# Kernel optimization log

Hardware: AMD Instinct MI355X
Metric: run time of the kernel (lower is better)

Reference implementation:

```python
import jax, jax.numpy as jnp
import numpy as np

EMBED_DIM = 1024
NUM_HEADS = 16
HEAD_DIM = EMBED_DIM // NUM_HEADS
WINDOW = 128  # window_size: attend to [i-W, i+W]


def setup_inputs() -> dict:
    key = jax.random.key(0)
    ks = jax.random.split(key, 9)
    B, S, E = 4, 4096, EMBED_DIM
    s = 1.0 / np.sqrt(E)
    return {
        "x": jax.random.normal(ks[0], (B, S, E), jnp.float32),
        "Wq": jax.random.normal(ks[1], (E, E), jnp.float32) * s,
        "bq": jnp.zeros((E,), jnp.float32),
        "Wk": jax.random.normal(ks[2], (E, E), jnp.float32) * s,
        "bk": jnp.zeros((E,), jnp.float32),
        "Wv": jax.random.normal(ks[3], (E, E), jnp.float32) * s,
        "bv": jnp.zeros((E,), jnp.float32),
        "Wo": jax.random.normal(ks[4], (E, E), jnp.float32) * s,
        "bo": jnp.zeros((E,), jnp.float32),
    }


def reference(x, Wq, bq, Wk, bk, Wv, bv, Wo, bo):
    B, S, E = x.shape
    H, D, W = NUM_HEADS, HEAD_DIM, WINDOW
    scale = jnp.sqrt(jnp.asarray(D, x.dtype))

    def heads(t):  # [B,S,E] -> [B,H,S,D]
        return t.reshape(B, S, H, D).transpose(0, 2, 1, 3)

    q = heads(x @ Wq + bq)
    k = heads(x @ Wk + bk)
    v = heads(x @ Wv + bv)

    # window indices per query position: j = i + [-W..W], masked to [0, S)
    offs = jnp.arange(-W, W + 1)                 # [2W+1]
    idx = jnp.arange(S)[:, None] + offs[None, :]  # [S, 2W+1]
    valid = (idx >= 0) & (idx < S)
    idxc = jnp.clip(idx, 0, S - 1)

    k_win = k[:, :, idxc, :]  # [B,H,S,2W+1,D]
    v_win = v[:, :, idxc, :]

    scores = jnp.einsum('bhsd,bhswd->bhsw', q, k_win) / scale
    scores = jnp.where(valid[None, None], scores, jnp.asarray(-jnp.inf, scores.dtype))
    attn = jax.nn.softmax(scores, axis=-1)
    out = jnp.einsum('bhsw,bhswd->bhsd', attn, v_win)  # [B,H,S,D]

    out = out.transpose(0, 2, 1, 3).reshape(B, S, E)
    return out @ Wo + bo
```

## Files before the change

kernel.cpp:

```cpp
#include <hip/hip_runtime.h>
#include <hip/hip_bf16.h>
#include <type_traits>

typedef unsigned short u16;
typedef __attribute__((ext_vector_type(8))) short  s16x8;
typedef __attribute__((ext_vector_type(4))) short  s16x4;
typedef __attribute__((ext_vector_type(8))) __bf16 b16x8;
typedef __attribute__((ext_vector_type(4))) float  f32x4;

#define S_LEN 4096
#define NB    4
#define EMB   1024
#define NH    16
#define HD    64
#define NROWS (NB * S_LEN)
#define KDIM  1024
#define BHSTRIDE (S_LEN * HD)

static __device__ __forceinline__ u16 f2b(float f) {
  __hip_bfloat16 h = __float2bfloat16(f);
  return __builtin_bit_cast(u16, h);
}

template <typename T, typename = void>
struct mfma_takes : std::false_type {};
template <typename T>
struct mfma_takes<T, std::void_t<decltype(__builtin_amdgcn_mfma_f32_16x16x32_bf16(
    std::declval<T>(), std::declval<T>(), std::declval<f32x4>(), 0, 0, 0))>> : std::true_type {};

template <typename AB>
static __device__ __forceinline__ f32x4 mfma_any(AB a, AB b, f32x4 c) {
  return __builtin_amdgcn_mfma_f32_16x16x32_bf16(a, b, c, 0, 0, 0);
}

template <typename S8 = s16x8, typename B8 = b16x8>
static __device__ __forceinline__ f32x4 MFMA_BF16(s16x8 a, s16x8 b, f32x4 c) {
  if constexpr (mfma_takes<S8>::value)
    return mfma_any<S8>(__builtin_bit_cast(S8, a), __builtin_bit_cast(S8, b), c);
  else
    return mfma_any<B8>(__builtin_bit_cast(B8, a), __builtin_bit_cast(B8, b), c);
}

static __device__ __forceinline__ void gld_lds16(const void* g, void* l) {
  __builtin_amdgcn_global_load_lds((const __attribute__((address_space(1))) void*)g,
                                   (__attribute__((address_space(3))) void*)l, 16, 0, 0);
}

__global__ __launch_bounds__(256) void cvt_x_kernel(const float* __restrict__ in,
                                                    u16* __restrict__ out) {
  long i = ((long)blockIdx.x * 256 + threadIdx.x) * 8;
  float4 a = *(const float4*)(in + i);
  float4 b = *(const float4*)(in + i + 4);
  s16x8 o;
  o[0] = (short)f2b(a.x); o[1] = (short)f2b(a.y); o[2] = (short)f2b(a.z); o[3] = (short)f2b(a.w);
  o[4] = (short)f2b(b.x); o[5] = (short)f2b(b.y); o[6] = (short)f2b(b.z); o[7] = (short)f2b(b.w);
  *(s16x8*)(out + i) = o;
}

__global__ __launch_bounds__(256) void transpose_cvt4_kernel(
    const float* __restrict__ W0, const float* __restrict__ W1,
    const float* __restrict__ W2, const float* __restrict__ W3,
    u16* __restrict__ D0, u16* __restrict__ D1, u16* __restrict__ D2, u16* __restrict__ D3) {
  __shared__ float tile[32][33];
  const float* W; u16* D;
  switch (blockIdx.z) {
    case 0:  W = W0; D = D0; break;
    case 1:  W = W1; D = D1; break;
    case 2:  W = W2; D = D2; break;
    default: W = W3; D = D3; break;
  }
  int n0 = blockIdx.x * 32, k0 = blockIdx.y * 32;
  int tx = threadIdx.x & 31, ty = threadIdx.x >> 5;
#pragma unroll
  for (int i = ty; i < 32; i += 8)
    tile[i][tx] = W[(long)(k0 + i) * EMB + n0 + tx];
  __syncthreads();
#pragma unroll
  for (int i = ty; i < 32; i += 8)
    D[(long)(n0 + i) * EMB + k0 + tx] = f2b(tile[tx][i]);
}

#define SA_(p,k) (((p)*2+(k))*8192)
#define SB_(p,k) (32768 + ((p)*2+(k))*8192)

__global__ __launch_bounds__(512, 2) void gemm8p_kernel(
    const u16* __restrict__ A, const u16* __restrict__ Bt,
    const float* __restrict__ b0, const float* __restrict__ b1, const float* __restrict__ b2,
    void* __restrict__ Cp, u16* __restrict__ Qb, u16* __restrict__ Kp, u16* __restrict__ Vt,
    int N, int out_f32) {
  __shared__ __align__(16) u16 smem[65536];
  const int tid = threadIdx.x;
  const int w = tid >> 6, lane = tid & 63;
  const int wm = w >> 2, wn = w & 3;
  const int frow = lane & 15, fg = lane >> 4;

  const int nwg = gridDim.x;
  const int bid = ((int)blockIdx.x & 7) * (nwg >> 3) + ((int)blockIdx.x >> 3);
  const int nbn = N >> 8;
  const int bm = bid / nbn, bn = bid % nbn;

  int offA[8];
#pragma unroll
  for (int j = 0; j < 8; j++) {
    int row = wm * 128 + j * 16 + frow;
    offA[j] = row * 32 + ((fg ^ ((row ^ (row >> 2)) & 3)) << 3);
  }
  int offB[4];
#pragma unroll
  for (int j = 0; j < 4; j++) {
    int row = wn * 64 + j * 16 + frow;
    offB[j] = row * 32 + ((fg ^ ((row ^ (row >> 2)) & 3)) << 3);
  }
  int srow[2], soff[2];
#pragma unroll
  for (int L = 0; L < 2; L++) {
    int lin = L * 512 + tid;
    int r = lin >> 2;
    srow[L] = r;
    soff[L] = (((lin & 3) ^ ((r ^ (r >> 2)) & 3)) << 3);
  }
  const u16* Abase = A + (long)bm * 256 * KDIM;
  const u16* Bbase = Bt + (long)bn * 256 * KDIM;

  f32x4 acc[8][4];
#pragma unroll
  for (int m = 0; m < 8; m++)
#pragma unroll
    for (int n = 0; n < 4; n++) acc[m][n] = (f32x4)0.0f;

  auto STAGE = [&](const u16* gb, int kcol, int slot) {
#pragma unroll
    for (int L = 0; L < 2; L++)
      gld_lds16(gb + (long)srow[L] * KDIM + kcol + soff[L],
                &smem[slot + (L * 512 + w * 64) * 8]);
  };

  s16x8 af[4], bf[4];

  STAGE(Abase, 0,  SA_(0,0)); STAGE(Bbase, 0,  SB_(0,0));
  STAGE(Abase, 32, SA_(0,1)); STAGE(Bbase, 32, SB_(0,1));
  STAGE(Abase, 64, SA_(1,0)); STAGE(Bbase, 64, SB_(1,0));
  asm volatile("s_waitcnt vmcnt(4)" ::: "memory");
  asm volatile("s_barrier" ::: "memory");

#define PHASE(p, k, mh, RDB, GB, KCOL, SLOT, DOVM)                            \
  {                                                                           \
    if (RDB) {                                                                \
      _Pragma("unroll") for (int n = 0; n < 4; n++)                           \
        bf[n] = *(const s16x8*)&smem[SB_(p, k) + offB[n]];                    \
    }                                                                         \
    _Pragma("unroll") for (int m = 0; m < 4; m++)                             \
      af[m] = *(const s16x8*)&smem[SA_(p, k) + offA[(mh) * 4 + m]];           \
    STAGE(GB, KCOL, SLOT);                                                    \
    asm volatile("s_barrier" ::: "memory");                                   \
    asm volatile("s_waitcnt lgkmcnt(0)" ::: "memory");                        \
    __builtin_amdgcn_sched_barrier(0);                                        \
    __builtin_amdgcn_s_setprio(1);                                            \
    _Pragma("unroll") for (int m = 0; m < 4; m++)                             \
      _Pragma("unroll") for (int n = 0; n < 4; n++)                           \
        acc[(mh) * 4 + m][n] = MFMA_BF16(af[m], bf[n], acc[(mh) * 4 + m][n]); \
    __builtin_amdgcn_s_setprio(0);                                            \
    if (DOVM) asm volatile("s_waitcnt vmcnt(4)" ::: "memory");                \
    asm volatile("s_barrier" ::: "memory");                                   \
  }

#pragma unroll 1
  for (int i = 0; i < 8; i++) {
    const int t = 2 * i;
    const int k1 = ((t + 1) & 15) * 64;
    const int k2 = ((t + 2) & 15) * 64;
    const int k3 = ((t + 3) & 15) * 64;
    PHASE(0, 0, 0, 1, Abase, k1 + 32, SA_(1, 1), 0)
    PHASE(0, 0, 1, 0, Bbase, k1 + 32, SB_(1, 1), 0)
    PHASE(0, 1, 0, 1, Abase, k2,      SA_(0, 0), 0)
    PHASE(0, 1, 1, 0, Bbase, k2,      SB_(0, 0), 1)
    PHASE(1, 0, 0, 1, Abase, k2 + 32, SA_(0, 1), 0)
    PHASE(1, 0, 1, 0, Bbase, k2 + 32, SB_(0, 1), 0)
    PHASE(1, 1, 0, 1, Abase, k3,      SA_(1, 0), 0)
    PHASE(1, 1, 1, 0, Bbase, k3,      SB_(1, 0), 1)
  }
#undef PHASE

  asm volatile("s_waitcnt vmcnt(0)" ::: "memory");
  asm volatile("s_barrier" ::: "memory");

  const int Mbase = bm * 256 + wm * 128;

  if (!out_f32) {
    const int g = bn * 256 + wn * 64;
    const int part = g >> 10;
    const int head = (g & 1023) >> 6;
    const float* bias = (part == 0) ? b0 : ((part == 1) ? b1 : b2);
    float bv[4];
#pragma unroll
    for (int n = 0; n < 4; n++) bv[n] = bias[(g & 1023) + n * 16 + frow];
    u16* buf = &smem[w * 2048];
#pragma unroll
    for (int mf2 = 0; mf2 < 4; mf2++) {
#pragma unroll
      for (int half = 0; half < 2; half++) {
        const int mf = mf2 * 2 + half;
#pragma unroll
        for (int n = 0; n < 4; n++)
#pragma unroll
          for (int r = 0; r < 4; r++) {
            int row32 = half * 16 + 4 * fg + r;
            int col = n * 16 + frow;
            buf[row32 * 64 + (((col >> 3) ^ (row32 & 7)) << 3) + (col & 7)] =
                f2b(acc[mf][n][r] + bv[n]);
          }
      }
      asm volatile("s_waitcnt lgkmcnt(0)" ::: "memory");
      __builtin_amdgcn_sched_barrier(0);
      const int s0 = Mbase + mf2 * 32;
      if (part == 2) {
        const int d = lane;
        u16 tmp[32];
#pragma unroll
        for (int r32 = 0; r32 < 32; r32++)
          tmp[r32] = buf[r32 * 64 + (((d >> 3) ^ (r32 & 7)) << 3) + (d & 7)];
        u16* dst = Vt + ((long)((s0 >> 12) * 16 + head)) * BHSTRIDE + (long)d * S_LEN + (s0 & 4095);
#pragma unroll
        for (int q = 0; q < 4; q++) {
          s16x8 pk;
#pragma unroll
          for (int j = 0; j < 8; j++) pk[j] = (short)tmp[q * 8 + j];
          *(s16x8*)(dst + q * 8) = pk;
        }
      } else {
#pragma unroll
        for (int i = 0; i < 4; i++) {
          int flat = lane + 64 * i;
          int row32 = flat >> 3, ch = flat & 7;
          s16x8 v = *(const s16x8*)&buf[row32 * 64 + ((ch ^ (row32 & 7)) << 3)];
          int s = s0 + row32;
          u16* dst = (part == 0)
              ? (Qb + (long)s * 1024 + head * 64 + ch * 8)
              : (Kp + ((long)(s >> 12) * 16 + head) * BHSTRIDE + (long)(s & 4095) * 64 + ch * 8);
          *(s16x8*)dst = v;
        }
      }
      asm volatile("s_waitcnt lgkmcnt(0)" ::: "memory");
      __builtin_amdgcn_sched_barrier(0);
    }
  } else {
    float* fbuf = (float*)&smem[w * 2048];
    const long crow0 = (long)Mbase * N + bn * 256 + wn * 64;
#pragma unroll
    for (int mf = 0; mf < 8; mf++) {
#pragma unroll
      for (int n = 0; n < 4; n++) {
        float bvv = b0[(bn * 256 + wn * 64 + n * 16 + frow) & 1023];
#pragma unroll
        for (int r = 0; r < 4; r++) {
          int row = 4 * fg + r;
          int o = 4 * n + (frow >> 2);
          fbuf[row * 64 + ((o ^ (row & 7)) << 2) + (frow & 3)] = acc[mf][n][r] + bvv;
        }
      }
      asm volatile("s_waitcnt lgkmcnt(0)" ::: "memory");
      __builtin_amdgcn_sched_barrier(0);
#pragma unroll
      for (int i = 0; i < 4; i++) {
        int flat = lane + 64 * i;
        int row = flat >> 4, oct = lane & 15;
        float4 v = *(const float4*)&fbuf[row * 64 + ((oct ^ (row & 7)) << 2)];
        *(float4*)((float*)Cp + crow0 + (long)(mf * 16 + row) * N + oct * 4) = v;
      }
      asm volatile("s_waitcnt lgkmcnt(0)" ::: "memory");
      __builtin_amdgcn_sched_barrier(0);
    }
  }
}

#define QBLK 128

__global__ __launch_bounds__(256) void attn_kernel(const u16* __restrict__ Qb,
                                                   const u16* __restrict__ Kp,
                                                   const u16* __restrict__ Vt,
                                                   u16* __restrict__ Oa) {
  __shared__ __align__(16) u16 smem[16384];

  const int tid = threadIdx.x;
  const int w = tid >> 6, lane = tid & 63;
  const int frow = lane & 15, fg = lane >> 4;

  const int nq = S_LEN / QBLK;
  int bid = (int)blockIdx.x;
  bid = (bid & 7) * ((NB * NH * nq) >> 3) + (bid >> 3);
  const int b = bid / (NH * nq);
  const int rem = bid % (NH * nq);
  const int h = rem / nq;
  const int qt = rem % nq;
  const int q0 = qt * QBLK;
  const int qw0 = q0 + 32 * w;

  const u16* Kpb = Kp + (long)(b * NH + h) * BHSTRIDE;
  const u16* Vtb = Vt + (long)(b * NH + h) * BHSTRIDE;

  s16x8 qf[2][2];
#pragma unroll
  for (int m = 0; m < 2; m++)
#pragma unroll
    for (int kk = 0; kk < 2; kk++)
      qf[m][kk] = *(const s16x8*)(Qb + (long)(b * S_LEN + qw0 + 16 * m + frow) * 1024 +
                                  h * 64 + kk * 32 + 8 * fg);

  f32x4 acc[2][4];
#pragma unroll
  for (int m = 0; m < 2; m++)
#pragma unroll
    for (int n = 0; n < 4; n++) acc[m][n] = (f32x4)0.0f;
  float mrow[2] = {-1e30f, -1e30f};
  float lrow[2] = {0.f, 0.f};

  const int r8 = lane >> 3;
  const int cs = ((lane & 7) ^ r8) << 3;

  auto STAGE = [&](int kvb, int bufi) {
#pragma unroll
    for (int pass = 0; pass < 2; pass++) {
      int rbase = pass * 32 + w * 8;
      gld_lds16(Kpb + (long)(kvb + rbase + r8) * 64 + cs, &smem[bufi * 4096 + rbase * 64]);
      gld_lds16(Vtb + (long)(rbase + r8) * S_LEN + kvb + cs, &smem[8192 + bufi * 4096 + rbase * 64]);
    }
  };

  const int tlo = (q0 == 0) ? 2 : 0;
  const int thi = (q0 == S_LEN - QBLK) ? 3 : 5;

  STAGE(q0 - 128 + 64 * tlo, 0);

#pragma unroll 1
  for (int t = tlo; t <= thi; t++) {
    const int cur = (t - tlo) & 1;
    const int kvb = q0 - 128 + 64 * t;
    if (t < thi) {
      STAGE(kvb + 64, cur ^ 1);
      asm volatile("s_waitcnt vmcnt(4)" ::: "memory");
    } else {
      asm volatile("s_waitcnt vmcnt(0)" ::: "memory");
    }
    asm volatile("s_barrier" ::: "memory");

    const bool active = (kvb + 63 >= qw0 - 128) && (kvb <= qw0 + 159);
    if (active) {
      const u16* lK = &smem[cur * 4096];
      const u16* lV = &smem[8192 + cur * 4096];
      f32x4 sfr[2][4];
#pragma unroll
      for (int m = 0; m < 2; m++)
#pragma unroll
        for (int n = 0; n < 4; n++) sfr[m][n] = (f32x4)0.0f;
#pragma unroll
      for (int kk = 0; kk < 2; kk++) {
        s16x8 kb[4];
#pragma unroll
        for (int n = 0; n < 4; n++)
          kb[n] = *(const s16x8*)&lK[(16 * n + frow) * 64 + (((fg + 4 * kk) ^ (frow & 7)) << 3)];
#pragma unroll
        for (int m = 0; m < 2; m++)
#pragma unroll
          for (int n = 0; n < 4; n++)
            sfr[m][n] = MFMA_BF16(kb[n], qf[m][kk], sfr[m][n]);
      }
#pragma unroll
      for (int m = 0; m < 2; m++) {
        const int q = qw0 + 16 * m + frow;
        float p[4][4];
        float tmax = -1e30f;
#pragma unroll
        for (int n = 0; n < 4; n++)
#pragma unroll
          for (int r = 0; r < 4; r++) {
            int kv = kvb + 16 * n + 4 * fg + r;
            bool valid = (kv >= q - 128) && (kv <= q + 128) && (kv >= 0) && (kv < S_LEN);
            float xv = valid ? sfr[m][n][r] * 0.125f : -1e30f;
            p[n][r] = xv;
            tmax = fmaxf(tmax, xv);
          }
        tmax = fmaxf(tmax, __shfl_xor(tmax, 16));
        tmax = fmaxf(tmax, __shfl_xor(tmax, 32));
        float mold = mrow[m];
        float mnew = fmaxf(mold, tmax);
        float al = __expf(mold - mnew);
        mrow[m] = mnew;
        float ps = 0.f;
#pragma unroll
        for (int n = 0; n < 4; n++)
#pragma unroll
          for (int r = 0; r < 4; r++) {
            float e = (p[n][r] > -1e29f) ? __expf(p[n][r] - mnew) : 0.f;
            p[n][r] = e;
            ps += e;
          }
        ps += __shfl_xor(ps, 16);
        ps += __shfl_xor(ps, 32);
        lrow[m] = lrow[m] * al + ps;
        float a4[4];
#pragma unroll
        for (int r = 0; r < 4; r++) a4[r] = __shfl(al, 20 * fg + r);
#pragma unroll
        for (int nd = 0; nd < 4; nd++)
#pragma unroll
          for (int r = 0; r < 4; r++) acc[m][nd][r] *= a4[r];
#pragma unroll
        for (int kt = 0; kt < 2; kt++) {
          s16x8 pa;
#pragma unroll
          for (int j = 0; j < 8; j++)
            pa[j] = (short)f2b(p[2 * kt + (j >> 2)][j & 3]);
#pragma unroll
          for (int nd = 0; nd < 4; nd++) {
            const int d = 16 * nd + frow;
            const int key = frow & 7;
            const int olo = (4 * kt + (fg >> 1)) ^ key;
            const int ohi = (4 * kt + 2 + (fg >> 1)) ^ key;
            s16x4 lo = *(const s16x4*)&lV[d * 64 + olo * 8 + (fg & 1) * 4];
            s16x4 hi = *(const s16x4*)&lV[d * 64 + ohi * 8 + (fg & 1) * 4];
            s16x8 vb;
            vb[0] = lo[0]; vb[1] = lo[1]; vb[2] = lo[2]; vb[3] = lo[3];
            vb[4] = hi[0]; vb[5] = hi[1]; vb[6] = hi[2]; vb[7] = hi[3];
            acc[m][nd] = MFMA_BF16(pa, vb, acc[m][nd]);
          }
        }
      }
    }
    asm volatile("s_barrier" ::: "memory");
  }

  float i4[2][4];
#pragma unroll
  for (int m = 0; m < 2; m++) {
    float inv = 1.0f / lrow[m];
#pragma unroll
    for (int r = 0; r < 4; r++) i4[m][r] = __shfl(inv, 20 * fg + r);
  }
  u16* bb = &smem[w * 2048];
#pragma unroll
  for (int m = 0; m < 2; m++)
#pragma unroll
    for (int nd = 0; nd < 4; nd++)
#pragma unroll
      for (int r = 0; r < 4; r++) {
        int row32 = 16 * m + 4 * fg + r;
        int col = 16 * nd + frow;
        bb[row32 * 64 + (((col >> 3) ^ (row32 & 7)) << 3) + (col & 7)] =
            f2b(acc[m][nd][r] * i4[m][r]);
      }
  asm volatile("s_waitcnt lgkmcnt(0)" ::: "memory");
  __builtin_amdgcn_sched_barrier(0);
  u16* Ob = Oa + ((long)(b * S_LEN + qw0)) * EMB + h * HD;
#pragma unroll
  for (int i = 0; i < 4; i++) {
    int flat = lane + 64 * i;
    int row32 = flat >> 3, ch = flat & 7;
    s16x8 v = *(const s16x8*)&bb[row32 * 64 + ((ch ^ (row32 & 7)) << 3)];
    *(s16x8*)(Ob + (long)row32 * EMB + ch * 8) = v;
  }
}

extern "C" void kernel_launch(void* const* d_in, const int* in_sizes, int n_in,
                              void* d_out, int out_size, void* d_ws, size_t ws_size,
                              hipStream_t stream) {
  const float* x  = (const float*)d_in[0];
  const float* Wq = (const float*)d_in[1];
  const float* bq = (const float*)d_in[2];
  const float* Wk = (const float*)d_in[3];
  const float* bk = (const float*)d_in[4];
  const float* Wv = (const float*)d_in[5];
  const float* bv = (const float*)d_in[6];
  const float* Wo = (const float*)d_in[7];
  const float* bo = (const float*)d_in[8];

  char* ws = (char*)d_ws;
  u16* xb   = (u16*)ws;  ws += (size_t)NROWS * EMB * 2;
  u16* Wt   = (u16*)ws;  ws += (size_t)3 * EMB * EMB * 2;
  u16* Wot  = (u16*)ws;  ws += (size_t)EMB * EMB * 2;
  u16* Qbuf = (u16*)ws;  ws += (size_t)NROWS * EMB * 2;
  u16* Kpb  = (u16*)ws;  ws += (size_t)NB * NH * BHSTRIDE * 2;
  u16* Vtb  = (u16*)ws;  ws += (size_t)NB * NH * BHSTRIDE * 2;
  u16* Oab  = (u16*)ws;  ws += (size_t)NROWS * EMB * 2;

  cvt_x_kernel<<<(NROWS * EMB) / (256 * 8), 256, 0, stream>>>(x, xb);

  dim3 tg(EMB / 32, EMB / 32, 4);
  transpose_cvt4_kernel<<<tg, 256, 0, stream>>>(
      Wq, Wk, Wv, Wo, Wt, Wt + (size_t)EMB * EMB, Wt + (size_t)2 * EMB * EMB, Wot);

  gemm8p_kernel<<<(NROWS / 256) * (3 * EMB / 256), 512, 0, stream>>>(
      xb, Wt, bq, bk, bv, nullptr, Qbuf, Kpb, Vtb, 3 * EMB, 0);

  attn_kernel<<<NB * NH * (S_LEN / QBLK), 256, 0, stream>>>(Qbuf, Kpb, Vtb, Oab);

  gemm8p_kernel<<<(NROWS / 256) * (EMB / 256), 512, 0, stream>>>(
      Oab, Wot, bo, bo, bo, d_out, nullptr, nullptr, nullptr, EMB, 1);
}
```

Before: 275.5 us.

## Double-buffer LDS fragment registers to prefetch next phase during MFMA

The GEMM main loop now keeps two register sets for the A and B fragments. Each phase issues the LDS reads for the next phase and then runs MFMAs on the previous phase's fragments, waiting only on partial lgkmcnt instead of draining to zero. The intent is to hide LDS read latency behind the matrix math. The cost is more VGPRs, which could reduce occupancy, and the barrier and vmcnt accounting becomes fragile, which risks data races.

After: 278.3 us. No clear change (+1.0%).

```diff
diff --git a/kernel.cpp b/kernel.cpp
--- a/kernel.cpp
+++ b/kernel.cpp
@@ -135,32 +135,37 @@
                 &smem[slot + (L * 512 + w * 64) * 8]);
   };
 
-  s16x8 af[4], bf[4];
+  s16x8 af[2][4], bfr[2][4];
 
   STAGE(Abase, 0,  SA_(0,0)); STAGE(Bbase, 0,  SB_(0,0));
   STAGE(Abase, 32, SA_(0,1)); STAGE(Bbase, 32, SB_(0,1));
   STAGE(Abase, 64, SA_(1,0)); STAGE(Bbase, 64, SB_(1,0));
-  asm volatile("s_waitcnt vmcnt(4)" ::: "memory");
+  asm volatile("s_waitcnt vmcnt(8)" ::: "memory");
   asm volatile("s_barrier" ::: "memory");
-
-#define PHASE(p, k, mh, RDB, GB, KCOL, SLOT, DOVM)                            \
+#pragma unroll
+  for (int n = 0; n < 4; n++) bfr[0][n] = *(const s16x8*)&smem[SB_(0,0) + offB[n]];
+#pragma unroll
+  for (int m = 0; m < 4; m++) af[0][m] = *(const s16x8*)&smem[SA_(0,0) + offA[m]];
+
+#define PH(PN, KN, MHN, RDB, AW, BW, GB, KCOL, SLOT, VM, MHC, AU, BU, LGN)    \
   {                                                                           \
     if (RDB) {                                                                \
       _Pragma("unroll") for (int n = 0; n < 4; n++)                           \
-        bf[n] = *(const s16x8*)&smem[SB_(p, k) + offB[n]];                    \
+        bfr[BW][n] = *(const s16x8*)&smem[SB_(PN, KN) + offB[n]];             \
     }                                                                         \
     _Pragma("unroll") for (int m = 0; m < 4; m++)                             \
-      af[m] = *(const s16x8*)&smem[SA_(p, k) + offA[(mh) * 4 + m]];           \
+      af[AW][m] = *(const s16x8*)&smem[SA_(PN, KN) + offA[(MHN) * 4 + m]];    \
     STAGE(GB, KCOL, SLOT);                                                    \
     asm volatile("s_barrier" ::: "memory");                                   \
-    asm volatile("s_waitcnt lgkmcnt(0)" ::: "memory");                        \
+    asm volatile("s_waitcnt lgkmcnt(" #LGN ")" ::: "memory");                 \
     __builtin_amdgcn_sched_barrier(0);                                        \
     __builtin_amdgcn_s_setprio(1);                                            \
     _Pragma("unroll") for (int m = 0; m < 4; m++)                             \
       _Pragma("unroll") for (int n = 0; n < 4; n++)                           \
-        acc[(mh) * 4 + m][n] = MFMA_BF16(af[m], bf[n], acc[(mh) * 4 + m][n]); \
+        acc[(MHC) * 4 + m][n] =                                               \
+            MFMA_BF16(af[AU][m], bfr[BU][n], acc[(MHC) * 4 + m][n]);          \
     __builtin_amdgcn_s_setprio(0);                                            \
-    if (DOVM) asm volatile("s_waitcnt vmcnt(4)" ::: "memory");                \
+    if (VM) asm volatile("s_waitcnt vmcnt(4)" ::: "memory");                  \
     asm volatile("s_barrier" ::: "memory");                                   \
   }
 
@@ -170,18 +175,18 @@
     const int k1 = ((t + 1) & 15) * 64;
     const int k2 = ((t + 2) & 15) * 64;
     const int k3 = ((t + 3) & 15) * 64;
-    PHASE(0, 0, 0, 1, Abase, k1 + 32, SA_(1, 1), 0)
-    PHASE(0, 0, 1, 0, Bbase, k1 + 32, SB_(1, 1), 0)
-    PHASE(0, 1, 0, 1, Abase, k2,      SA_(0, 0), 0)
-    PHASE(0, 1, 1, 0, Bbase, k2,      SB_(0, 0), 1)
-    PHASE(1, 0, 0, 1, Abase, k2 + 32, SA_(0, 1), 0)
-    PHASE(1, 0, 1, 0, Bbase, k2 + 32, SB_(0, 1), 0)
-    PHASE(1, 1, 0, 1, Abase, k3,      SA_(1, 0), 0)
-    PHASE(1, 1, 1, 0, Bbase, k3,      SB_(1, 0), 1)
-  }
-#undef PHASE
-
-  asm volatile("s_waitcnt vmcnt(0)" ::: "memory");
+    PH(0, 0, 1, 0, 1, 0, Abase, k1 + 32, SA_(1, 1), 0, 0, 0, 0, 4)
+    PH(0, 1, 0, 1, 0, 1, Bbase, k1 + 32, SB_(1, 1), 1, 1, 1, 0, 8)
+    PH(0, 1, 1, 0, 1, 0, Abase, k2,      SA_(0, 0), 0, 0, 0, 1, 4)
+    PH(1, 0, 0, 1, 0, 0, Bbase, k2,      SB_(0, 0), 1, 1, 1, 1, 8)
+    PH(1, 0, 1, 0, 1, 0, Abase, k2 + 32, SA_(0, 1), 0, 0, 0, 0, 4)
+    PH(1, 1, 0, 1, 0, 1, Bbase, k2 + 32, SB_(0, 1), 1, 1, 1, 0, 8)
+    PH(1, 1, 1, 0, 1, 0, Abase, k3,      SA_(1, 0), 0, 0, 0, 1, 4)
+    PH(0, 0, 0, 1, 0, 0, Bbase, k3,      SB_(1, 0), 1, 1, 1, 1, 8)
+  }
+#undef PH
+
+  asm volatile("s_waitcnt vmcnt(0) lgkmcnt(0)" ::: "memory");
   asm volatile("s_barrier" ::: "memory");
 
   const int Mbase = bm * 256 + wm * 128;
```
